# Kernel tuning notes

Measured on AMD Instinct MI355X. Metric: run time of the kernel, lower is better.

The kernel has to match this reference:

```python
import jax, jax.numpy as jnp
import numpy as np

B, C, N = 4, 192, 4096
K = 16                      # avg degree
E = B * N * K               # 262144 edges
C_OUT = 384


def setup_inputs() -> dict:
    key = jax.random.key(0)
    k1, k2, k3, k4 = jax.random.split(key, 4)
    x = jax.random.normal(k1, (B, C, N, 1), dtype=jnp.float32)
    edge_index = jax.random.randint(k2, (2, E), 0, B * N, dtype=jnp.int64)
    # BasicConv([2C, C_OUT]): 1x1 Conv2d + bias + ReLU (norm=None)
    W = jax.random.normal(k3, (C_OUT, 2 * C), dtype=jnp.float32) * (1.0 / np.sqrt(2 * C))
    b = jax.random.normal(k4, (C_OUT,), dtype=jnp.float32) * 0.01
    return {"x": x, "edge_index": edge_index, "W": W, "b": b}


def reference(x, edge_index, W, b):
    Bs, Cs, Ns, _ = x.shape
    BN = Bs * Ns
    # (B,C,N,1) -> flattened node table (B*N, C); node id = b*N + n
    x_flat = jnp.transpose(x[..., 0], (0, 2, 1)).reshape(BN, Cs)
    x_i = x_flat[edge_index[0]]          # (E, C) gather at dst
    x_j = x_flat[edge_index[1]]          # (E, C) gather at src
    diff = x_j - x_i
    # scatter-max over dst nodes; torch_scatter fills empty segments with 0
    agg = jax.ops.segment_max(diff, edge_index[0], num_segments=BN)
    agg = jnp.where(jnp.isfinite(agg), agg, 0.0)
    x_j_out = jnp.transpose(agg.reshape(Bs, Ns, Cs), (0, 2, 1))[..., None]  # (B,C,N,1)
    # interleave channels: cat along new axis 2 then reshape -> (B, 2C, N, 1)
    cat = jnp.stack([x, x_j_out], axis=2).reshape(Bs, 2 * Cs, Ns, 1)
    # 1x1 conv == GEMM over channels, + bias + ReLU
    out = jnp.einsum('oc,bcnw->bonw', W, cat) + b[None, :, None, None]
    return jax.nn.relu(out)
```

## Files before the change

kernel.cpp:

```cpp
#include <hip/hip_runtime.h>
#include <hip/hip_bf16.h>
#include <math.h>

#define Bz    4
#define Cch   192
#define Nn    4096
#define BN    16384
#define Ecnt  262144
#define COUT  384
#define CAP   64

typedef __attribute__((ext_vector_type(8))) short short8;
typedef __attribute__((ext_vector_type(4))) float floatx4;

__device__ __forceinline__ void gload_lds16(const void* g, void* l) {
    __builtin_amdgcn_global_load_lds(
        (const __attribute__((address_space(1))) unsigned int*)g,
        (__attribute__((address_space(3))) unsigned int*)l, 16, 0, 0);
}

__device__ __forceinline__ float b2f(unsigned short u) {
    union { unsigned int i; float f; } z; z.i = ((unsigned int)u) << 16; return z.f;
}
__device__ __forceinline__ unsigned short f2b(float f) {
    __hip_bfloat16 h = __float2bfloat16(f);
    return *(unsigned short*)&h;
}

__global__ __launch_bounds__(256) void prep_kernel(
    const float* __restrict__ x, const unsigned int* __restrict__ ew,
    const float* __restrict__ W, __hip_bfloat16* __restrict__ xb,
    __hip_bfloat16* __restrict__ Wxa, __hip_bfloat16* __restrict__ Wa,
    int* __restrict__ deg, int* __restrict__ flag) {
    int bid = blockIdx.x;
    if (bid < 3072) {
        __shared__ float tile[32][33];
        int b = bid / 768;
        int r = bid - b * 768;
        int c0 = (r >> 7) * 32;
        int n0 = (r & 127) * 32;
        int tx = threadIdx.x & 31, ty = threadIdx.x >> 5;
        for (int i = ty; i < 32; i += 8)
            tile[i][tx] = x[((size_t)(b * Cch + c0 + i)) * Nn + n0 + tx];
        __syncthreads();
        for (int i = ty; i < 32; i += 8)
            xb[((size_t)(b * Nn + n0 + i)) * Cch + c0 + tx] =
                __float2bfloat16(tile[tx][i]);
    } else if (bid < 3360) {
        int i = (bid - 3072) * 256 + threadIdx.x;
        int o = i / Cch, c = i - o * Cch;
        float wx = W[o * 2 * Cch + 2 * c];
        float wa = W[o * 2 * Cch + 2 * c + 1];
        Wxa[i] = __float2bfloat16(wx - wa);
        Wa[i]  = __float2bfloat16(wa);
    } else if (bid < 3424) {
        deg[(bid - 3360) * 256 + threadIdx.x] = 0;
    } else {
        __shared__ int s;
        if (threadIdx.x == 0) s = 1;
        __syncthreads();
        if (ew[2 * threadIdx.x + 1] != 0u) atomicAnd(&s, 0);
        __syncthreads();
        if (threadIdx.x == 0) *flag = s;
    }
}

__global__ __launch_bounds__(256) void fill_kernel(
    const int* __restrict__ ew, const int* __restrict__ flag,
    int* __restrict__ deg, int* __restrict__ slots) {
    int t = blockIdx.x * 256 + threadIdx.x;
    int d0, d1, s0, s1;
    if (*flag) {
        int4 dv = *(const int4*)&ew[4 * t];
        int4 sv = *(const int4*)&ew[2 * Ecnt + 4 * t];
        d0 = dv.x; d1 = dv.z; s0 = sv.x; s1 = sv.z;
    } else {
        int2 dv = *(const int2*)&ew[2 * t];
        int2 sv = *(const int2*)&ew[Ecnt + 2 * t];
        d0 = dv.x; d1 = dv.y; s0 = sv.x; s1 = sv.y;
    }
    int p0 = atomicAdd(&deg[d0], 1); if (p0 < CAP) slots[(d0 << 6) + p0] = s0;
    int p1 = atomicAdd(&deg[d1], 1); if (p1 < CAP) slots[(d1 << 6) + p1] = s1;
}

#define RED8(mm, FLD) do {                                                    \
    float a_ = fmaxf(fmaxf(b2f(v[0].FLD), b2f(v[1].FLD)),                     \
                     fmaxf(b2f(v[2].FLD), b2f(v[3].FLD)));                    \
    float b_ = fmaxf(fmaxf(b2f(v[4].FLD), b2f(v[5].FLD)),                     \
                     fmaxf(b2f(v[6].FLD), b2f(v[7].FLD)));                    \
    mm = fmaxf(mm, fmaxf(a_, b_)); } while (0)

__global__ __launch_bounds__(256) void agg_kernel(
    const int* __restrict__ deg, const int* __restrict__ slots,
    const __hip_bfloat16* __restrict__ xb, __hip_bfloat16* __restrict__ Mb) {
    int lane = threadIdx.x & 63, wave = threadIdx.x >> 6;
    int node = (blockIdx.x << 2) + wave;
    int d = deg[node]; if (d > CAP) d = CAP;
    d = __builtin_amdgcn_readfirstlane(d);
    int nbrval = 0;
    if (lane < d) nbrval = slots[(node << 6) + lane];
    const unsigned short* xbu = (const unsigned short*)xb;
    int act = lane < 48;
    int cb = lane * 4;
    float m0 = -INFINITY, m1 = -INFINITY, m2 = -INFINITY, m3 = -INFINITY;
    int k = 0;
    for (; k + 8 <= d; k += 8) {
        int s[8];
#pragma unroll
        for (int u = 0; u < 8; u++) s[u] = __builtin_amdgcn_readlane(nbrval, k + u);
        if (act) {
            ushort4 v[8];
#pragma unroll
            for (int u = 0; u < 8; u++) v[u] = *(const ushort4*)&xbu[s[u] * Cch + cb];
            RED8(m0, x); RED8(m1, y); RED8(m2, z); RED8(m3, w);
        }
    }
    if (k + 4 <= d) {
        int s0 = __builtin_amdgcn_readlane(nbrval, k);
        int s1 = __builtin_amdgcn_readlane(nbrval, k + 1);
        int s2 = __builtin_amdgcn_readlane(nbrval, k + 2);
        int s3 = __builtin_amdgcn_readlane(nbrval, k + 3);
        if (act) {
            ushort4 v0 = *(const ushort4*)&xbu[s0 * Cch + cb];
            ushort4 v1 = *(const ushort4*)&xbu[s1 * Cch + cb];
            ushort4 v2 = *(const ushort4*)&xbu[s2 * Cch + cb];
            ushort4 v3 = *(const ushort4*)&xbu[s3 * Cch + cb];
            m0 = fmaxf(m0, fmaxf(fmaxf(b2f(v0.x), b2f(v1.x)), fmaxf(b2f(v2.x), b2f(v3.x))));
            m1 = fmaxf(m1, fmaxf(fmaxf(b2f(v0.y), b2f(v1.y)), fmaxf(b2f(v2.y), b2f(v3.y))));
            m2 = fmaxf(m2, fmaxf(fmaxf(b2f(v0.z), b2f(v1.z)), fmaxf(b2f(v2.z), b2f(v3.z))));
            m3 = fmaxf(m3, fmaxf(fmaxf(b2f(v0.w), b2f(v1.w)), fmaxf(b2f(v2.w), b2f(v3.w))));
        }
        k += 4;
    }
    for (; k < d; k++) {
        int s = __builtin_amdgcn_readlane(nbrval, k);
        if (act) {
            ushort4 v = *(const ushort4*)&xbu[s * Cch + cb];
            m0 = fmaxf(m0, b2f(v.x)); m1 = fmaxf(m1, b2f(v.y));
            m2 = fmaxf(m2, b2f(v.z)); m3 = fmaxf(m3, b2f(v.w));
        }
    }
    if (act) {
        ushort4 o4;
        if (d > 0) {
            o4.x = f2b(m0); o4.y = f2b(m1); o4.z = f2b(m2); o4.w = f2b(m3);
        } else {
            o4 = *(const ushort4*)&xbu[node * Cch + cb];
        }
        *(ushort4*)&((unsigned short*)Mb)[node * Cch + cb] = o4;
    }
}

__global__ __launch_bounds__(256) void gemm_kernel(
    const __hip_bfloat16* __restrict__ Xb, const __hip_bfloat16* __restrict__ Ab,
    const __hip_bfloat16* __restrict__ Wxa, const __hip_bfloat16* __restrict__ Wa,
    const float* __restrict__ bias, float* __restrict__ out) {
    __shared__ short As[2][64 * 32];
    __shared__ short Bs[2][128 * 32];
    int t = threadIdx.x;
    int node0 = blockIdx.x * 64;
    int o0    = blockIdx.y * 128;
    int lane = t & 63, wave = t >> 6;
    int quad = lane >> 4, lrow = lane & 15;
    int wm = wave & 1, wn = wave >> 1;

    floatx4 acc[2][4] = {};
    int srow = t >> 2;
    int koff = (t & 3) * 8;

    size_t aoff = (size_t)(node0 + srow) * Cch + koff;
    size_t boff = (size_t)(o0 + srow) * Cch + koff;
    const __hip_bfloat16* Ag[2] = {Xb + aoff, Ab + aoff};
    const __hip_bfloat16* Bg[2] = {Wxa + boff, Wa + boff};

    auto STAGE = [&](int s, int b) {
        int seg = (s >= 6);
        int kt = (seg ? s - 6 : s) * 32;
        gload_lds16(Ag[seg] + kt, &As[b][t * 8]);
        gload_lds16(Bg[seg] + kt, &Bs[b][t * 8]);
        gload_lds16(Bg[seg] + (size_t)64 * Cch + kt, &Bs[b][2048 + t * 8]);
    };

    STAGE(0, 0);
    __syncthreads();
    for (int s = 0; s < 12; s++) {
        int p = s & 1;
        if (s < 11) STAGE(s + 1, p ^ 1);
        short8 af[2], bf[4];
#pragma unroll
        for (int i = 0; i < 2; i++)
            af[i] = *(const short8*)&As[p][(wm * 32 + i * 16 + lrow) * 32 + quad * 8];
#pragma unroll
        for (int j = 0; j < 4; j++)
            bf[j] = *(const short8*)&Bs[p][(wn * 64 + j * 16 + lrow) * 32 + quad * 8];
#pragma unroll
        for (int i = 0; i < 2; i++)
#pragma unroll
            for (int j = 0; j < 4; j++)
                acc[i][j] = __builtin_amdgcn_mfma_f32_16x16x32_bf16(bf[j], af[i], acc[i][j], 0, 0, 0);
        __syncthreads();
    }

#pragma unroll
    for (int i = 0; i < 2; i++) {
        int node = node0 + wm * 32 + i * 16 + lrow;
        int b = node >> 12, n = node & 4095;
#pragma unroll
        for (int j = 0; j < 4; j++) {
            int ob = o0 + wn * 64 + j * 16 + quad * 4;
#pragma unroll
            for (int r = 0; r < 4; r++) {
                int o = ob + r;
                float v = acc[i][j][r] + bias[o];
                out[((size_t)(b * COUT + o)) * Nn + n] = fmaxf(v, 0.0f);
            }
        }
    }
}

extern "C" void kernel_launch(void* const* d_in, const int* in_sizes, int n_in,
                              void* d_out, int out_size, void* d_ws, size_t ws_size,
                              hipStream_t stream) {
    const float* x    = (const float*)d_in[0];
    const int*   ew   = (const int*)d_in[1];
    const float* W    = (const float*)d_in[2];
    const float* bias = (const float*)d_in[3];
    float* out        = (float*)d_out;

    char* ws = (char*)d_ws;
    __hip_bfloat16* xb   = (__hip_bfloat16*)ws;
    __hip_bfloat16* Mb   = (__hip_bfloat16*)(ws + 6291456);
    __hip_bfloat16* Wxa  = (__hip_bfloat16*)(ws + 12582912);
    __hip_bfloat16* Wa   = (__hip_bfloat16*)(ws + 12730368);
    int* deg   = (int*)(ws + 12877824);
    int* slots = (int*)(ws + 12943360);
    int* flag  = (int*)(ws + 17137664);

    prep_kernel<<<3425, 256, 0, stream>>>(x, (const unsigned int*)ew, W, xb, Wxa, Wa, deg, flag);
    fill_kernel<<<Ecnt / 512, 256, 0, stream>>>(ew, flag, deg, slots);
    agg_kernel<<<BN / 4, 256, 0, stream>>>(deg, slots, xb, Mb);
    gemm_kernel<<<dim3(BN / 64, COUT / 128), 256, 0, stream>>>(xb, Mb, Wxa, Wa, bias, out);
}
```

Measured before the change: 115.5 us.

## Fuse neighbor max-aggregation into GEMM kernel via shared-memory aggregate tile

```diff
diff --git a/kernel.cpp b/kernel.cpp
--- a/kernel.cpp
+++ b/kernel.cpp
@@ -9,6 +9,7 @@
 #define Ecnt  262144
 #define COUT  384
 #define CAP   64
+#define MSTR  200
 
 typedef __attribute__((ext_vector_type(8))) short short8;
 typedef __attribute__((ext_vector_type(4))) float floatx4;
@@ -90,124 +91,130 @@
                      fmaxf(b2f(v[6].FLD), b2f(v[7].FLD)));                    \
     mm = fmaxf(mm, fmaxf(a_, b_)); } while (0)
 
-__global__ __launch_bounds__(256) void agg_kernel(
+__global__ __launch_bounds__(256) void fused_kernel(
     const int* __restrict__ deg, const int* __restrict__ slots,
-    const __hip_bfloat16* __restrict__ xb, __hip_bfloat16* __restrict__ Mb) {
-    int lane = threadIdx.x & 63, wave = threadIdx.x >> 6;
-    int node = (blockIdx.x << 2) + wave;
-    int d = deg[node]; if (d > CAP) d = CAP;
-    d = __builtin_amdgcn_readfirstlane(d);
-    int nbrval = 0;
-    if (lane < d) nbrval = slots[(node << 6) + lane];
+    const __hip_bfloat16* __restrict__ xb,
+    const __hip_bfloat16* __restrict__ Wxa, const __hip_bfloat16* __restrict__ Wa,
+    const float* __restrict__ bias, float* __restrict__ out) {
+    __shared__ unsigned short Ms[32 * MSTR];
+    __shared__ short As[2][128 * 8];
+    __shared__ short Bs[2][1536 * 8];
+    int t = threadIdx.x;
+    int lane = t & 63, wave = t >> 6;
+    int quad = lane >> 4, lrow = lane & 15;
+    int node0 = blockIdx.x * 32;
     const unsigned short* xbu = (const unsigned short*)xb;
+
+    auto STAGE = [&](int skt, int bf_) {
+        const __hip_bfloat16* Wseg = (skt >= 6) ? Wa : Wxa;
+        int kt = ((skt >= 6) ? skt - 6 : skt) * 32;
+#pragma unroll
+        for (int m = 0; m < 6; m++) {
+            int o = m * 64 + lane;
+            gload_lds16(Wseg + (size_t)o * Cch + kt + wave * 8,
+                        &Bs[bf_][(wave * 384 + o) * 8]);
+        }
+        if (skt < 6 && wave < 2) {
+            int c = wave * 64 + lane;
+            int q = c >> 5, nd = c & 31;
+            gload_lds16(xb + (size_t)(node0 + nd) * Cch + kt + q * 8,
+                        &As[bf_][c * 8]);
+        }
+    };
+
+    STAGE(0, 0);
+
     int act = lane < 48;
     int cb = lane * 4;
-    float m0 = -INFINITY, m1 = -INFINITY, m2 = -INFINITY, m3 = -INFINITY;
-    int k = 0;
-    for (; k + 8 <= d; k += 8) {
-        int s[8];
-#pragma unroll
-        for (int u = 0; u < 8; u++) s[u] = __builtin_amdgcn_readlane(nbrval, k + u);
+    for (int nl = wave * 8; nl < wave * 8 + 8; nl++) {
+        int node = node0 + nl;
+        int d = deg[node]; if (d > CAP) d = CAP;
+        d = __builtin_amdgcn_readfirstlane(d);
+        int nbrval = 0;
+        if (lane < d) nbrval = slots[(node << 6) + lane];
+        float m0 = -INFINITY, m1 = -INFINITY, m2 = -INFINITY, m3 = -INFINITY;
+        int k = 0;
+        for (; k + 8 <= d; k += 8) {
+            int s[8];
+#pragma unroll
+            for (int u = 0; u < 8; u++) s[u] = __builtin_amdgcn_readlane(nbrval, k + u);
+            if (act) {
+                ushort4 v[8];
+#pragma unroll
+                for (int u = 0; u < 8; u++) v[u] = *(const ushort4*)&xbu[s[u] * Cch + cb];
+                RED8(m0, x); RED8(m1, y); RED8(m2, z); RED8(m3, w);
+            }
+        }
+        if (k + 4 <= d) {
+            int s0 = __builtin_amdgcn_readlane(nbrval, k);
+            int s1 = __builtin_amdgcn_readlane(nbrval, k + 1);
+            int s2 = __builtin_amdgcn_readlane(nbrval, k + 2);
+            int s3 = __builtin_amdgcn_readlane(nbrval, k + 3);
+            if (act) {
+                ushort4 v0 = *(const ushort4*)&xbu[s0 * Cch + cb];
+                ushort4 v1 = *(const ushort4*)&xbu[s1 * Cch + cb];
+                ushort4 v2 = *(const ushort4*)&xbu[s2 * Cch + cb];
+                ushort4 v3 = *(const ushort4*)&xbu[s3 * Cch + cb];
+                m0 = fmaxf(m0, fmaxf(fmaxf(b2f(v0.x), b2f(v1.x)), fmaxf(b2f(v2.x), b2f(v3.x))));
+                m1 = fmaxf(m1, fmaxf(fmaxf(b2f(v0.y), b2f(v1.y)), fmaxf(b2f(v2.y), b2f(v3.y))));
+                m2 = fmaxf(m2, fmaxf(fmaxf(b2f(v0.z), b2f(v1.z)), fmaxf(b2f(v2.z), b2f(v3.z))));
+                m3 = fmaxf(m3, fmaxf(fmaxf(b2f(v0.w), b2f(v1.w)), fmaxf(b2f(v2.w), b2f(v3.w))));
+            }
+            k += 4;
+        }
+        for (; k < d; k++) {
+            int s = __builtin_amdgcn_readlane(nbrval, k);
+            if (act) {
+                ushort4 v = *(const ushort4*)&xbu[s * Cch + cb];
+                m0 = fmaxf(m0, b2f(v.x)); m1 = fmaxf(m1, b2f(v.y));
+                m2 = fmaxf(m2, b2f(v.z)); m3 = fmaxf(m3, b2f(v.w));
+            }
+        }
         if (act) {
-            ushort4 v[8];
-#pragma unroll
-            for (int u = 0; u < 8; u++) v[u] = *(const ushort4*)&xbu[s[u] * Cch + cb];
-            RED8(m0, x); RED8(m1, y); RED8(m2, z); RED8(m3, w);
-        }
-    }
-    if (k + 4 <= d) {
-        int s0 = __builtin_amdgcn_readlane(nbrval, k);
-        int s1 = __builtin_amdgcn_readlane(nbrval, k + 1);
-        int s2 = __builtin_amdgcn_readlane(nbrval, k + 2);
-        int s3 = __builtin_amdgcn_readlane(nbrval, k + 3);
-        if (act) {
-            ushort4 v0 = *(const ushort4*)&xbu[s0 * Cch + cb];
-            ushort4 v1 = *(const ushort4*)&xbu[s1 * Cch + cb];
-            ushort4 v2 = *(const ushort4*)&xbu[s2 * Cch + cb];
-            ushort4 v3 = *(const ushort4*)&xbu[s3 * Cch + cb];
-            m0 = fmaxf(m0, fmaxf(fmaxf(b2f(v0.x), b2f(v1.x)), fmaxf(b2f(v2.x), b2f(v3.x))));
-            m1 = fmaxf(m1, fmaxf(fmaxf(b2f(v0.y), b2f(v1.y)), fmaxf(b2f(v2.y), b2f(v3.y))));
-            m2 = fmaxf(m2, fmaxf(fmaxf(b2f(v0.z), b2f(v1.z)), fmaxf(b2f(v2.z), b2f(v3.z))));
-            m3 = fmaxf(m3, fmaxf(fmaxf(b2f(v0.w), b2f(v1.w)), fmaxf(b2f(v2.w), b2f(v3.w))));
-        }
-        k += 4;
-    }
-    for (; k < d; k++) {
-        int s = __builtin_amdgcn_readlane(nbrval, k);
-        if (act) {
-            ushort4 v = *(const ushort4*)&xbu[s * Cch + cb];
-            m0 = fmaxf(m0, b2f(v.x)); m1 = fmaxf(m1, b2f(v.y));
-            m2 = fmaxf(m2, b2f(v.z)); m3 = fmaxf(m3, b2f(v.w));
-        }
-    }
-    if (act) {
-        ushort4 o4;
-        if (d > 0) {
-            o4.x = f2b(m0); o4.y = f2b(m1); o4.z = f2b(m2); o4.w = f2b(m3);
-        } else {
-            o4 = *(const ushort4*)&xbu[node * Cch + cb];
-        }
-        *(ushort4*)&((unsigned short*)Mb)[node * Cch + cb] = o4;
-    }
-}
-
-__global__ __launch_bounds__(256) void gemm_kernel(
-    const __hip_bfloat16* __restrict__ Xb, const __hip_bfloat16* __restrict__ Ab,
-    const __hip_bfloat16* __restrict__ Wxa, const __hip_bfloat16* __restrict__ Wa,
-    const float* __restrict__ bias, float* __restrict__ out) {
-    __shared__ short As[2][64 * 32];
-    __shared__ short Bs[2][128 * 32];
-    int t = threadIdx.x;
-    int node0 = blockIdx.x * 64;
-    int o0    = blockIdx.y * 128;
-    int lane = t & 63, wave = t >> 6;
-    int quad = lane >> 4, lrow = lane & 15;
-    int wm = wave & 1, wn = wave >> 1;
-
-    floatx4 acc[2][4] = {};
-    int srow = t >> 2;
-    int koff = (t & 3) * 8;
-
-    size_t aoff = (size_t)(node0 + srow) * Cch + koff;
-    size_t boff = (size_t)(o0 + srow) * Cch + koff;
-    const __hip_bfloat16* Ag[2] = {Xb + aoff, Ab + aoff};
-    const __hip_bfloat16* Bg[2] = {Wxa + boff, Wa + boff};
-
-    auto STAGE = [&](int s, int b) {
-        int seg = (s >= 6);
-        int kt = (seg ? s - 6 : s) * 32;
-        gload_lds16(Ag[seg] + kt, &As[b][t * 8]);
-        gload_lds16(Bg[seg] + kt, &Bs[b][t * 8]);
-        gload_lds16(Bg[seg] + (size_t)64 * Cch + kt, &Bs[b][2048 + t * 8]);
-    };
-
-    STAGE(0, 0);
+            ushort4 o4;
+            if (d > 0) {
+                o4.x = f2b(m0); o4.y = f2b(m1); o4.z = f2b(m2); o4.w = f2b(m3);
+            } else {
+                o4 = *(const ushort4*)&xbu[node * Cch + cb];
+            }
+            *(ushort4*)&Ms[nl * MSTR + cb] = o4;
+        }
+    }
     __syncthreads();
+
+    floatx4 acc[2][6] = {};
     for (int s = 0; s < 12; s++) {
         int p = s & 1;
         if (s < 11) STAGE(s + 1, p ^ 1);
-        short8 af[2], bf[4];
+        short8 af[2], bf[6];
+        if (s < 6) {
+#pragma unroll
+            for (int i = 0; i < 2; i++)
+                af[i] = *(const short8*)&As[p][(quad * 32 + i * 16 + lrow) * 8];
+        } else {
+            int kk = (s - 6) * 32 + quad * 8;
+#pragma unroll
+            for (int i = 0; i < 2; i++)
+                af[i] = *(const short8*)&Ms[(i * 16 + lrow) * MSTR + kk];
+        }
+#pragma unroll
+        for (int j = 0; j < 6; j++)
+            bf[j] = *(const short8*)&Bs[p][(quad * 384 + wave * 96 + j * 16 + lrow) * 8];
 #pragma unroll
         for (int i = 0; i < 2; i++)
-            af[i] = *(const short8*)&As[p][(wm * 32 + i * 16 + lrow) * 32 + quad * 8];
-#pragma unroll
-        for (int j = 0; j < 4; j++)
-            bf[j] = *(const short8*)&Bs[p][(wn * 64 + j * 16 + lrow) * 32 + quad * 8];
-#pragma unroll
-        for (int i = 0; i < 2; i++)
-#pragma unroll
-            for (int j = 0; j < 4; j++)
+#pragma unroll
+            for (int j = 0; j < 6; j++)
                 acc[i][j] = __builtin_amdgcn_mfma_f32_16x16x32_bf16(bf[j], af[i], acc[i][j], 0, 0, 0);
         __syncthreads();
     }
 
 #pragma unroll
     for (int i = 0; i < 2; i++) {
-        int node = node0 + wm * 32 + i * 16 + lrow;
+        int node = node0 + i * 16 + lrow;
         int b = node >> 12, n = node & 4095;
 #pragma unroll
-        for (int j = 0; j < 4; j++) {
-            int ob = o0 + wn * 64 + j * 16 + quad * 4;
+        for (int j = 0; j < 6; j++) {
+            int ob = wave * 96 + j * 16 + quad * 4;
 #pragma unroll
             for (int r = 0; r < 4; r++) {
                 int o = ob + r;
@@ -229,7 +236,6 @@
 
     char* ws = (char*)d_ws;
     __hip_bfloat16* xb   = (__hip_bfloat16*)ws;
-    __hip_bfloat16* Mb   = (__hip_bfloat16*)(ws + 6291456);
     __hip_bfloat16* Wxa  = (__hip_bfloat16*)(ws + 12582912);
     __hip_bfloat16* Wa   = (__hip_bfloat16*)(ws + 12730368);
     int* deg   = (int*)(ws + 12877824);
@@ -238,6 +244,5 @@
 
     prep_kernel<<<3425, 256, 0, stream>>>(x, (const unsigned int*)ew, W, xb, Wxa, Wa, deg, flag);
     fill_kernel<<<Ecnt / 512, 256, 0, stream>>>(ew, flag, deg, slots);
-    agg_kernel<<<BN / 4, 256, 0, stream>>>(deg, slots, xb, Mb);
-    gemm_kernel<<<dim3(BN / 64, COUT / 128), 256, 0, stream>>>(xb, Mb, Wxa, Wa, bias, out);
-}
+    fused_kernel<<<BN / 32, 256, 0, stream>>>(deg, slots, xb, Wxa, Wa, bias, out);
+}
```

New measurement: 135.5 us. +17.3%, slower.

## Fuse edge fill into prep kernel and widen aggregation unroll to 16

Applied to the files above, without the earlier changes.

```diff
diff --git a/kernel.cpp b/kernel.cpp
--- a/kernel.cpp
+++ b/kernel.cpp
@@ -27,11 +27,30 @@
     return *(unsigned short*)&h;
 }
 
-__global__ __launch_bounds__(256) void prep_kernel(
-    const float* __restrict__ x, const unsigned int* __restrict__ ew,
-    const float* __restrict__ W, __hip_bfloat16* __restrict__ xb,
+#define RED8(mm, FLD) do {                                                    \
+    float a_ = fmaxf(fmaxf(b2f(v[0].FLD), b2f(v[1].FLD)),                     \
+                     fmaxf(b2f(v[2].FLD), b2f(v[3].FLD)));                    \
+    float b_ = fmaxf(fmaxf(b2f(v[4].FLD), b2f(v[5].FLD)),                     \
+                     fmaxf(b2f(v[6].FLD), b2f(v[7].FLD)));                    \
+    mm = fmaxf(mm, fmaxf(a_, b_)); } while (0)
+
+#define RED16(mm, FLD) do {                                                   \
+    float a_ = fmaxf(fmaxf(fmaxf(b2f(v[0].FLD), b2f(v[1].FLD)),               \
+                           fmaxf(b2f(v[2].FLD), b2f(v[3].FLD))),              \
+                     fmaxf(fmaxf(b2f(v[4].FLD), b2f(v[5].FLD)),               \
+                           fmaxf(b2f(v[6].FLD), b2f(v[7].FLD))));             \
+    float b_ = fmaxf(fmaxf(fmaxf(b2f(v[8].FLD), b2f(v[9].FLD)),               \
+                           fmaxf(b2f(v[10].FLD), b2f(v[11].FLD))),            \
+                     fmaxf(fmaxf(b2f(v[12].FLD), b2f(v[13].FLD)),             \
+                           fmaxf(b2f(v[14].FLD), b2f(v[15].FLD))));           \
+    mm = fmaxf(mm, fmaxf(a_, b_)); } while (0)
+
+template <int IS64>
+__global__ __launch_bounds__(256) void combo_kernel(
+    const float* __restrict__ x, const float* __restrict__ W,
+    const int* __restrict__ ew, __hip_bfloat16* __restrict__ xb,
     __hip_bfloat16* __restrict__ Wxa, __hip_bfloat16* __restrict__ Wa,
-    int* __restrict__ deg, int* __restrict__ flag) {
+    int* __restrict__ deg, int* __restrict__ slots) {
     int bid = blockIdx.x;
     if (bid < 3072) {
         __shared__ float tile[32][33];
@@ -53,57 +72,50 @@
         float wa = W[o * 2 * Cch + 2 * c + 1];
         Wxa[i] = __float2bfloat16(wx - wa);
         Wa[i]  = __float2bfloat16(wa);
-    } else if (bid < 3424) {
-        deg[(bid - 3360) * 256 + threadIdx.x] = 0;
     } else {
-        __shared__ int s;
-        if (threadIdx.x == 0) s = 1;
-        __syncthreads();
-        if (ew[2 * threadIdx.x + 1] != 0u) atomicAnd(&s, 0);
-        __syncthreads();
-        if (threadIdx.x == 0) *flag = s;
-    }
-}
-
-__global__ __launch_bounds__(256) void fill_kernel(
-    const int* __restrict__ ew, const int* __restrict__ flag,
-    int* __restrict__ deg, int* __restrict__ slots) {
-    int t = blockIdx.x * 256 + threadIdx.x;
-    int d0, d1, s0, s1;
-    if (*flag) {
-        int4 dv = *(const int4*)&ew[4 * t];
-        int4 sv = *(const int4*)&ew[2 * Ecnt + 4 * t];
-        d0 = dv.x; d1 = dv.z; s0 = sv.x; s1 = sv.z;
-    } else {
-        int2 dv = *(const int2*)&ew[2 * t];
-        int2 sv = *(const int2*)&ew[Ecnt + 2 * t];
-        d0 = dv.x; d1 = dv.y; s0 = sv.x; s1 = sv.y;
-    }
-    int p0 = atomicAdd(&deg[d0], 1); if (p0 < CAP) slots[(d0 << 6) + p0] = s0;
-    int p1 = atomicAdd(&deg[d1], 1); if (p1 < CAP) slots[(d1 << 6) + p1] = s1;
-}
-
-#define RED8(mm, FLD) do {                                                    \
-    float a_ = fmaxf(fmaxf(b2f(v[0].FLD), b2f(v[1].FLD)),                     \
-                     fmaxf(b2f(v[2].FLD), b2f(v[3].FLD)));                    \
-    float b_ = fmaxf(fmaxf(b2f(v[4].FLD), b2f(v[5].FLD)),                     \
-                     fmaxf(b2f(v[6].FLD), b2f(v[7].FLD)));                    \
-    mm = fmaxf(mm, fmaxf(a_, b_)); } while (0)
+        int t = (bid - 3360) * 256 + threadIdx.x;
+        int d0, d1, s0, s1;
+        if (IS64) {
+            int4 dv = *(const int4*)&ew[4 * t];
+            int4 sv = *(const int4*)&ew[2 * Ecnt + 4 * t];
+            d0 = dv.x; d1 = dv.z; s0 = sv.x; s1 = sv.z;
+        } else {
+            int2 dv = *(const int2*)&ew[2 * t];
+            int2 sv = *(const int2*)&ew[Ecnt + 2 * t];
+            d0 = dv.x; d1 = dv.y; s0 = sv.x; s1 = sv.y;
+        }
+        int p0 = atomicAdd(&deg[d0], 1); if (p0 < CAP) slots[(d0 << 6) + p0] = s0;
+        int p1 = atomicAdd(&deg[d1], 1); if (p1 < CAP) slots[(d1 << 6) + p1] = s1;
+    }
+}
 
 __global__ __launch_bounds__(256) void agg_kernel(
     const int* __restrict__ deg, const int* __restrict__ slots,
     const __hip_bfloat16* __restrict__ xb, __hip_bfloat16* __restrict__ Mb) {
     int lane = threadIdx.x & 63, wave = threadIdx.x >> 6;
     int node = (blockIdx.x << 2) + wave;
-    int d = deg[node]; if (d > CAP) d = CAP;
-    d = __builtin_amdgcn_readfirstlane(d);
-    int nbrval = 0;
-    if (lane < d) nbrval = slots[(node << 6) + lane];
+    int d = deg[node];
+    int nbrval = slots[(node << 6) + lane];
     const unsigned short* xbu = (const unsigned short*)xb;
     int act = lane < 48;
     int cb = lane * 4;
+    ushort4 xv = {0, 0, 0, 0};
+    if (act) xv = *(const ushort4*)&xbu[node * Cch + cb];
+    if (d > CAP) d = CAP;
+    d = __builtin_amdgcn_readfirstlane(d);
     float m0 = -INFINITY, m1 = -INFINITY, m2 = -INFINITY, m3 = -INFINITY;
     int k = 0;
+    for (; k + 16 <= d; k += 16) {
+        int s[16];
+#pragma unroll
+        for (int u = 0; u < 16; u++) s[u] = __builtin_amdgcn_readlane(nbrval, k + u);
+        if (act) {
+            ushort4 v[16];
+#pragma unroll
+            for (int u = 0; u < 16; u++) v[u] = *(const ushort4*)&xbu[s[u] * Cch + cb];
+            RED16(m0, x); RED16(m1, y); RED16(m2, z); RED16(m3, w);
+        }
+    }
     for (; k + 8 <= d; k += 8) {
         int s[8];
 #pragma unroll
@@ -114,23 +126,6 @@
             for (int u = 0; u < 8; u++) v[u] = *(const ushort4*)&xbu[s[u] * Cch + cb];
             RED8(m0, x); RED8(m1, y); RED8(m2, z); RED8(m3, w);
         }
-    }
-    if (k + 4 <= d) {
-        int s0 = __builtin_amdgcn_readlane(nbrval, k);
-        int s1 = __builtin_amdgcn_readlane(nbrval, k + 1);
-        int s2 = __builtin_amdgcn_readlane(nbrval, k + 2);
-        int s3 = __builtin_amdgcn_readlane(nbrval, k + 3);
-        if (act) {
-            ushort4 v0 = *(const ushort4*)&xbu[s0 * Cch + cb];
-            ushort4 v1 = *(const ushort4*)&xbu[s1 * Cch + cb];
-            ushort4 v2 = *(const ushort4*)&xbu[s2 * Cch + cb];
-            ushort4 v3 = *(const ushort4*)&xbu[s3 * Cch + cb];
-            m0 = fmaxf(m0, fmaxf(fmaxf(b2f(v0.x), b2f(v1.x)), fmaxf(b2f(v2.x), b2f(v3.x))));
-            m1 = fmaxf(m1, fmaxf(fmaxf(b2f(v0.y), b2f(v1.y)), fmaxf(b2f(v2.y), b2f(v3.y))));
-            m2 = fmaxf(m2, fmaxf(fmaxf(b2f(v0.z), b2f(v1.z)), fmaxf(b2f(v2.z), b2f(v3.z))));
-            m3 = fmaxf(m3, fmaxf(fmaxf(b2f(v0.w), b2f(v1.w)), fmaxf(b2f(v2.w), b2f(v3.w))));
-        }
-        k += 4;
     }
     for (; k < d; k++) {
         int s = __builtin_amdgcn_readlane(nbrval, k);
@@ -145,7 +140,7 @@
         if (d > 0) {
             o4.x = f2b(m0); o4.y = f2b(m1); o4.z = f2b(m2); o4.w = f2b(m3);
         } else {
-            o4 = *(const ushort4*)&xbu[node * Cch + cb];
+            o4 = xv;
         }
         *(ushort4*)&((unsigned short*)Mb)[node * Cch + cb] = o4;
     }
@@ -234,10 +229,14 @@
     __hip_bfloat16* Wa   = (__hip_bfloat16*)(ws + 12730368);
     int* deg   = (int*)(ws + 12877824);
     int* slots = (int*)(ws + 12943360);
-    int* flag  = (int*)(ws + 17137664);
-
-    prep_kernel<<<3425, 256, 0, stream>>>(x, (const unsigned int*)ew, W, xb, Wxa, Wa, deg, flag);
-    fill_kernel<<<Ecnt / 512, 256, 0, stream>>>(ew, flag, deg, slots);
+
+    bool is64 = (in_sizes[1] >= (int)(2u * Ecnt * 8u));
+
+    hipMemsetAsync(deg, 0, BN * sizeof(int), stream);
+    if (is64)
+        combo_kernel<1><<<3872, 256, 0, stream>>>(x, W, ew, xb, Wxa, Wa, deg, slots);
+    else
+        combo_kernel<0><<<3872, 256, 0, stream>>>(x, W, ew, xb, Wxa, Wa, deg, slots);
     agg_kernel<<<BN / 4, 256, 0, stream>>>(deg, slots, xb, Mb);
     gemm_kernel<<<dim3(BN / 64, COUT / 128), 256, 0, stream>>>(xb, Mb, Wxa, Wa, bias, out);
 }
```

Measured after the change: 114.7 us. About the same (-0.8%).
